# Kernel optimization log

Measured on AMD Instinct MI355X. Metric: run time of the kernel, lower is better.

Reference implementation:

```python
import jax, jax.numpy as jnp
import numpy as np
from jax import lax

B, DIM, H, W = 32, 256, 56, 56
HID = 4 * DIM
EPS = 1e-6


def setup_inputs() -> dict:
    key = jax.random.key(0)
    ks = jax.random.split(key, 8)
    x = jax.random.normal(ks[0], (B, DIM, H, W), dtype=jnp.float32)
    # depthwise conv: OIHW with feature_group_count=DIM -> [DIM, 1, 7, 7]
    conv_w = jax.random.normal(ks[1], (DIM, 1, 7, 7), dtype=jnp.float32) * 0.05
    conv_b = jax.random.normal(ks[2], (DIM,), dtype=jnp.float32) * 0.01
    ln_g = jnp.ones((DIM,), dtype=jnp.float32)
    ln_b = jnp.zeros((DIM,), dtype=jnp.float32)
    w1 = jax.random.normal(ks[3], (DIM, HID), dtype=jnp.float32) * (1.0 / np.sqrt(DIM))
    b1 = jax.random.normal(ks[4], (HID,), dtype=jnp.float32) * 0.01
    w2 = jax.random.normal(ks[5], (HID, DIM), dtype=jnp.float32) * (1.0 / np.sqrt(HID))
    b2 = jax.random.normal(ks[6], (DIM,), dtype=jnp.float32) * 0.01
    return {"x": x, "conv_w": conv_w, "conv_b": conv_b, "ln_g": ln_g,
            "ln_b": ln_b, "w1": w1, "b1": b1, "w2": w2, "b2": b2}


def reference(x, conv_w, conv_b, ln_g, ln_b, w1, b1, w2, b2):
    dim = x.shape[1]
    # 7x7 depthwise conv, stride 1, padding 3 (NCHW)
    y = lax.conv_general_dilated(
        x, conv_w, window_strides=(1, 1), padding=((3, 3), (3, 3)),
        dimension_numbers=("NCHW", "OIHW", "NCHW"), feature_group_count=dim)
    y = y + conv_b[None, :, None, None]
    # permute to NHWC
    y = jnp.transpose(y, (0, 2, 3, 1))  # [B, H, W, C]
    # LayerNorm over channel (last) dim, eps=1e-6, affine
    mu = jnp.mean(y, axis=-1, keepdims=True)
    var = jnp.mean(jnp.square(y - mu), axis=-1, keepdims=True)
    y = (y - mu) * lax.rsqrt(var + EPS) * ln_g + ln_b
    # MLP: Linear -> exact GELU -> Linear
    h = jax.nn.gelu(jnp.einsum("bhwc,cf->bhwf", y, w1) + b1, approximate=False)
    y = jnp.einsum("bhwf,fc->bhwc", h, w2) + b2
    # permute back to NCHW; stochastic depth is identity at eval time
    return jnp.transpose(y, (0, 3, 1, 2))
```

## Files before the change

kernel.cpp:

```cpp
#include <hip/hip_runtime.h>
#include <math.h>

#define CDIM 256
#define HW 3136
#define HID 1024

typedef __attribute__((ext_vector_type(4))) float f32x4;
typedef __attribute__((ext_vector_type(8))) short bf16x8;
typedef __attribute__((ext_vector_type(4))) short bf16x4;

__device__ __forceinline__ unsigned short f2bf(float f){
  unsigned int u = __float_as_uint(f);
  u += 0x7FFFu + ((u >> 16) & 1u);
  return (unsigned short)(u >> 16);
}

__device__ __forceinline__ void load_lds16(const void* g, void* l){
  __builtin_amdgcn_global_load_lds(
      (const __attribute__((address_space(1))) unsigned int*)g,
      (__attribute__((address_space(3))) unsigned int*)l, 16, 0, 0);
}

__global__ __launch_bounds__(256) void prep_kernel(
    const float* __restrict__ w1, const float* __restrict__ w2,
    unsigned short* __restrict__ w1t, unsigned short* __restrict__ w2t){
  __shared__ unsigned short sh[64][70];
  int blk = blockIdx.x;
  const float* src; unsigned short* dst; int M, N, tm, tn;
  if (blk < 64){ src = w1; dst = w1t; M = 256;  N = 1024; tm = blk >> 4; tn = blk & 15; }
  else { blk -= 64; src = w2; dst = w2t; M = 1024; N = 256;  tm = blk >> 2; tn = blk & 3; }
  const int t = threadIdx.x;

  {
    const int r = t >> 4, c4 = t & 15;
    #pragma unroll
    for (int rr = 0; rr < 4; ++rr){
      int row = rr * 16 + r;
      f32x4 v = *(const f32x4*)(src + (long)(tm * 64 + row) * N + tn * 64 + c4 * 4);
      #pragma unroll
      for (int k = 0; k < 4; ++k) sh[row][c4 * 4 + k] = f2bf(v[k]);
    }
  }
  __syncthreads();

  {
    const int n = t >> 2, seg = t & 3;
    bf16x8 o0, o1;
    #pragma unroll
    for (int j = 0; j < 8; ++j){
      o0[j] = (short)sh[seg * 16 + j][n];
      o1[j] = (short)sh[seg * 16 + 8 + j][n];
    }
    unsigned short* dp = dst + (long)(tn * 64 + n) * M + tm * 64 + seg * 16;
    *(bf16x8*)(dp) = o0;
    *(bf16x8*)(dp + 8) = o1;
  }
}

__global__ __launch_bounds__(256) void convln_kernel(
    const float* __restrict__ x, const float* __restrict__ cw,
    const float* __restrict__ cb, const float* __restrict__ lng,
    const float* __restrict__ lnb, unsigned short* __restrict__ y){
  __shared__ float tile[256 * 61];
  __shared__ float part_s[4][64];
  __shared__ float part_q[4][64];
  __shared__ float lg_s[256];
  __shared__ float lb_s[256];

  const int t = threadIdx.x;
  const int blk = blockIdx.x;
  const int b = blk / 56;
  const int h = blk - b * 56;
  const int c = t;

  lg_s[t] = lng[t];
  lb_s[t] = lnb[t];

  float acc[56];
  {
    float bias = cb[c];
    #pragma unroll
    for (int w = 0; w < 56; ++w) acc[w] = bias;
  }

  const float* xim = x + (long)(b * 256 + c) * HW;
  const float* cwc = cw + c * 49;
  for (int i = 0; i < 7; ++i){
    int hh = h - 3 + i;
    if (hh >= 0 && hh < 56){
      float seg[62];
      seg[0] = seg[1] = seg[2] = 0.f;
      seg[59] = seg[60] = seg[61] = 0.f;
      const float* xrow = xim + hh * 56;
      #pragma unroll
      for (int w4 = 0; w4 < 14; ++w4){
        f32x4 v = *(const f32x4*)(xrow + w4 * 4);
        seg[3 + w4 * 4 + 0] = v[0];
        seg[3 + w4 * 4 + 1] = v[1];
        seg[3 + w4 * 4 + 2] = v[2];
        seg[3 + w4 * 4 + 3] = v[3];
      }
      float wt7[7];
      #pragma unroll
      for (int j = 0; j < 7; ++j) wt7[j] = cwc[i * 7 + j];
      #pragma unroll
      for (int j = 0; j < 7; ++j){
        float wj = wt7[j];
        #pragma unroll
        for (int w = 0; w < 56; ++w)
          acc[w] = fmaf(seg[w + j], wj, acc[w]);
      }
    }
  }

  #pragma unroll
  for (int p = 0; p < 56; ++p) tile[c * 61 + p] = acc[p];
  __syncthreads();

  {
    int p = t & 63; if (p > 55) p = 55;
    const int q = t >> 6;
    float s = 0.f, qq = 0.f;
    #pragma unroll 8
    for (int j = 0; j < 64; ++j){
      float v = tile[(q * 64 + j) * 61 + p];
      s += v; qq = fmaf(v, v, qq);
    }
    part_s[q][p] = s;
    part_q[q][p] = qq;
  }
  __syncthreads();

  if (t < 224){
    const int p = t >> 2, c0 = (t & 3) * 64;
    float S = part_s[0][p] + part_s[1][p] + part_s[2][p] + part_s[3][p];
    float Q = part_q[0][p] + part_q[1][p] + part_q[2][p] + part_q[3][p];
    float mu = S * (1.0f / 256.0f);
    float var = Q * (1.0f / 256.0f) - mu * mu;
    float rs = rsqrtf(var + 1e-6f);
    long pos = (long)blk * 56 + p;
    int m7 = (int)(pos & 7);
    unsigned short* yp = y + pos * 256 + c0;
    #pragma unroll
    for (int j = 0; j < 8; ++j){
      bf16x8 o;
      #pragma unroll
      for (int k = 0; k < 8; ++k){
        int cc = c0 + j * 8 + k;
        float v = tile[cc * 61 + p];
        o[k] = (short)f2bf((v - mu) * rs * lg_s[cc] + lb_s[cc]);
      }
      *(bf16x8*)(yp + (j ^ m7) * 8) = o;
    }
  }
}

#define LDS_H0 32768
#define MLP_LDS (32768 + 18432)

__global__ __launch_bounds__(256, 3) void mlp_kernel(
    const unsigned short* __restrict__ y, const unsigned short* __restrict__ w1t,
    const unsigned short* __restrict__ w2t, const float* __restrict__ b1,
    const float* __restrict__ b2, float* __restrict__ out){
  __shared__ __align__(16) unsigned char smem[MLP_LDS];
  const int t = threadIdx.x;
  const int wv = t >> 6, lane = t & 63;
  const int lr = lane & 15, lq = lane >> 4;
  const int r7 = lr & 7;
  const int blk = blockIdx.x;

  {
    const unsigned char* ybase = (const unsigned char*)(y + (long)blk * 64 * 256);
    #pragma unroll
    for (int r = 0; r < 8; ++r){
      int g = wv * 8 + r;
      load_lds16(ybase + g * 1024 + lane * 16, smem + g * 1024);
    }
  }

  f32x4 acc2[4][4];
  #pragma unroll
  for (int a = 0; a < 4; ++a)
    #pragma unroll
    for (int bb = 0; bb < 4; ++bb) acc2[a][bb] = (f32x4){0.f, 0.f, 0.f, 0.f};

  __syncthreads();

  for (int ch = 0; ch < 16; ++ch){
    unsigned char* Hbuf = smem + LDS_H0 + (ch & 1) * 9216;

    const unsigned short* w1p = w1t + (((long)ch * 64 + wv * 16 + lr) << 8);
    bf16x8 wf[8];
    #pragma unroll
    for (int ks = 0; ks < 8; ++ks)
      wf[ks] = *(const bf16x8*)(w1p + ks * 32 + lq * 8);

    f32x4 acc1[4];
    #pragma unroll
    for (int mt = 0; mt < 4; ++mt) acc1[mt] = (f32x4){0.f, 0.f, 0.f, 0.f};
    #pragma unroll
    for (int ks = 0; ks < 8; ++ks){
      bf16x8 yf[4];
      #pragma unroll
      for (int mt = 0; mt < 4; ++mt){
        int jl = ks * 4 + lq;
        int ofs = (mt * 16 + lr) * 512 + (((jl & 24) | ((jl ^ r7) & 7)) << 4);
        yf[mt] = *(const bf16x8*)(smem + ofs);
      }
      #pragma unroll
      for (int mt = 0; mt < 4; ++mt)
        acc1[mt] = __builtin_amdgcn_mfma_f32_16x16x32_bf16(wf[ks], yf[mt], acc1[mt], 0, 0, 0);
    }

    bf16x8 w2f[2][4];
    #pragma unroll
    for (int ks2 = 0; ks2 < 2; ++ks2)
      #pragma unroll
      for (int ct = 0; ct < 4; ++ct)
        w2f[ks2][ct] = *(const bf16x8*)(w2t + (long)(wv * 64 + ct * 16 + lr) * 1024
                                        + ch * 64 + ks2 * 32 + lq * 8);

    {
      f32x4 bv = *(const f32x4*)(b1 + ch * 64 + wv * 16 + lq * 4);
      #pragma unroll
      for (int mt = 0; mt < 4; ++mt){
        bf16x4 hv;
        #pragma unroll
        for (int r = 0; r < 4; ++r){
          float pv = acc1[mt][r] + bv[r];
          float p2 = pv * pv;
          float u  = pv * fmaf(0.044715f, p2, 1.0f);
          float e  = __builtin_amdgcn_exp2f(-2.3022083f * u);
          float gl = pv * __builtin_amdgcn_rcpf(1.0f + e);
          hv[r] = (short)f2bf(gl);
        }
        *(bf16x4*)(Hbuf + (mt * 16 + lr) * 144 + wv * 32 + lq * 8) = hv;
      }
    }
    __syncthreads();

    #pragma unroll
    for (int ks2 = 0; ks2 < 2; ++ks2){
      bf16x8 hf[4];
      #pragma unroll
      for (int mt = 0; mt < 4; ++mt)
        hf[mt] = *(const bf16x8*)(Hbuf + (mt * 16 + lr) * 144 + ks2 * 64 + lq * 16);
      #pragma unroll
      for (int ct = 0; ct < 4; ++ct)
        #pragma unroll
        for (int mt = 0; mt < 4; ++mt)
          acc2[ct][mt] = __builtin_amdgcn_mfma_f32_16x16x32_bf16(w2f[ks2][ct], hf[mt], acc2[ct][mt], 0, 0, 0);
    }
  }

  #pragma unroll
  for (int ct = 0; ct < 4; ++ct){
    int cb = wv * 64 + ct * 16 + lq * 4;
    f32x4 b2v = *(const f32x4*)(b2 + cb);
    #pragma unroll
    for (int mt = 0; mt < 4; ++mt){
      int m = mt * 16 + lr;
      unsigned pos = (unsigned)(blk * 64 + m);
      unsigned bimg = pos / 3136u;
      unsigned hw = pos - bimg * 3136u;
      float* op = out + ((long)bimg * 256 + cb) * 3136 + hw;
      #pragma unroll
      for (int r = 0; r < 4; ++r)
        op[r * 3136] = acc2[ct][mt][r] + b2v[r];
    }
  }
}

extern "C" void kernel_launch(void* const* d_in, const int* in_sizes, int n_in,
                              void* d_out, int out_size, void* d_ws, size_t ws_size,
                              hipStream_t stream){
  const float* x  = (const float*)d_in[0];
  const float* cw = (const float*)d_in[1];
  const float* cb = (const float*)d_in[2];
  const float* lg = (const float*)d_in[3];
  const float* lb = (const float*)d_in[4];
  const float* w1 = (const float*)d_in[5];
  const float* b1 = (const float*)d_in[6];
  const float* w2 = (const float*)d_in[7];
  const float* b2 = (const float*)d_in[8];
  float* out = (float*)d_out;

  unsigned short* y   = (unsigned short*)d_ws;
  unsigned short* w1t = (unsigned short*)((char*)d_ws + 51380224);
  unsigned short* w2t = (unsigned short*)((char*)d_ws + 51904512);

  hipLaunchKernelGGL(prep_kernel,   dim3(128),  dim3(256), 0, stream, w1, w2, w1t, w2t);
  hipLaunchKernelGGL(convln_kernel, dim3(1792), dim3(256), 0, stream, x, cw, cb, lg, lb, y);
  hipLaunchKernelGGL(mlp_kernel,    dim3(1568), dim3(256), 0, stream, y, w1t, w2t, b1, b2, out);
}
```

Measured before the change: 527.5 us.

## Stage conv rows through LDS and single-buffer swizzled MLP hidden tile

The conv kernel now loads each input row for all 256 channels into LDS cooperatively with coalesced 16-byte loads, and each thread reads its channel's row from LDS. Before, each thread loaded its own strided channel row straight from global memory. The MLP kernel replaces its padded double-buffered hidden tile with a single XOR-swizzled 8KB buffer. This lowers LDS use so four blocks can fit per CU instead of three, at the cost of an extra barrier per chunk. The conv path also gains two barriers per kernel row.

```diff
diff --git a/kernel.cpp b/kernel.cpp
--- a/kernel.cpp
+++ b/kernel.cpp
@@ -61,7 +61,7 @@
     const float* __restrict__ x, const float* __restrict__ cw,
     const float* __restrict__ cb, const float* __restrict__ lng,
     const float* __restrict__ lnb, unsigned short* __restrict__ y){
-  __shared__ float tile[256 * 61];
+  __shared__ float buf[256 * 61];
   __shared__ float part_s[4][64];
   __shared__ float part_q[4][64];
   __shared__ float lg_s[256];
@@ -83,22 +83,34 @@
     for (int w = 0; w < 56; ++w) acc[w] = bias;
   }
 
-  const float* xim = x + (long)(b * 256 + c) * HW;
+  const int sl = t & 15;
+  const int rg = t >> 4;
+  const float* xb = x + (long)b * 256 * HW;
   const float* cwc = cw + c * 49;
+
   for (int i = 0; i < 7; ++i){
     int hh = h - 3 + i;
     if (hh >= 0 && hh < 56){
+      __syncthreads();
+      if (sl < 14){
+        #pragma unroll 4
+        for (int k = 0; k < 16; ++k){
+          int cr = k * 16 + rg;
+          f32x4 v = *(const f32x4*)(xb + (long)cr * HW + hh * 56 + sl * 4);
+          *(f32x4*)(buf + cr * 57 + sl * 4) = v;
+        }
+      }
+      __syncthreads();
       float seg[62];
       seg[0] = seg[1] = seg[2] = 0.f;
       seg[59] = seg[60] = seg[61] = 0.f;
-      const float* xrow = xim + hh * 56;
-      #pragma unroll
-      for (int w4 = 0; w4 < 14; ++w4){
-        f32x4 v = *(const f32x4*)(xrow + w4 * 4);
-        seg[3 + w4 * 4 + 0] = v[0];
-        seg[3 + w4 * 4 + 1] = v[1];
-        seg[3 + w4 * 4 + 2] = v[2];
-        seg[3 + w4 * 4 + 3] = v[3];
+      #pragma unroll
+      for (int s4 = 0; s4 < 14; ++s4){
+        f32x4 v = *(const f32x4*)(buf + c * 57 + s4 * 4);
+        seg[3 + s4 * 4 + 0] = v[0];
+        seg[3 + s4 * 4 + 1] = v[1];
+        seg[3 + s4 * 4 + 2] = v[2];
+        seg[3 + s4 * 4 + 3] = v[3];
       }
       float wt7[7];
       #pragma unroll
@@ -113,8 +125,9 @@
     }
   }
 
+  __syncthreads();
   #pragma unroll
-  for (int p = 0; p < 56; ++p) tile[c * 61 + p] = acc[p];
+  for (int p = 0; p < 56; ++p) buf[c * 61 + p] = acc[p];
   __syncthreads();
 
   {
@@ -123,7 +136,7 @@
     float s = 0.f, qq = 0.f;
     #pragma unroll 8
     for (int j = 0; j < 64; ++j){
-      float v = tile[(q * 64 + j) * 61 + p];
+      float v = buf[(q * 64 + j) * 61 + p];
       s += v; qq = fmaf(v, v, qq);
     }
     part_s[q][p] = s;
@@ -147,7 +160,7 @@
       #pragma unroll
       for (int k = 0; k < 8; ++k){
         int cc = c0 + j * 8 + k;
-        float v = tile[cc * 61 + p];
+        float v = buf[cc * 61 + p];
         o[k] = (short)f2bf((v - mu) * rs * lg_s[cc] + lb_s[cc]);
       }
       *(bf16x8*)(yp + (j ^ m7) * 8) = o;
@@ -156,9 +169,9 @@
 }
 
 #define LDS_H0 32768
-#define MLP_LDS (32768 + 18432)
-
-__global__ __launch_bounds__(256, 3) void mlp_kernel(
+#define MLP_LDS (32768 + 8192)
+
+__global__ __launch_bounds__(256, 4) void mlp_kernel(
     const unsigned short* __restrict__ y, const unsigned short* __restrict__ w1t,
     const unsigned short* __restrict__ w2t, const float* __restrict__ b1,
     const float* __restrict__ b2, float* __restrict__ out){
@@ -168,6 +181,7 @@
   const int lr = lane & 15, lq = lane >> 4;
   const int r7 = lr & 7;
   const int blk = blockIdx.x;
+  unsigned char* Hbuf = smem + LDS_H0;
 
   {
     const unsigned char* ybase = (const unsigned char*)(y + (long)blk * 64 * 256);
@@ -187,8 +201,6 @@
   __syncthreads();
 
   for (int ch = 0; ch < 16; ++ch){
-    unsigned char* Hbuf = smem + LDS_H0 + (ch & 1) * 9216;
-
     const unsigned short* w1p = w1t + (((long)ch * 64 + wv * 16 + lr) << 8);
     bf16x8 wf[8];
     #pragma unroll
@@ -222,6 +234,8 @@
 
     {
       f32x4 bv = *(const f32x4*)(b1 + ch * 64 + wv * 16 + lq * 4);
+      const int j = wv * 2 + (lq >> 1);
+      const int half = lq & 1;
       #pragma unroll
       for (int mt = 0; mt < 4; ++mt){
         bf16x4 hv;
@@ -234,7 +248,8 @@
           float gl = pv * __builtin_amdgcn_rcpf(1.0f + e);
           hv[r] = (short)f2bf(gl);
         }
-        *(bf16x4*)(Hbuf + (mt * 16 + lr) * 144 + wv * 32 + lq * 8) = hv;
+        int off = (mt * 16 + lr) * 128 + (((j ^ r7)) << 4) + (half << 3);
+        *(bf16x4*)(Hbuf + off) = hv;
       }
     }
     __syncthreads();
@@ -243,14 +258,17 @@
     for (int ks2 = 0; ks2 < 2; ++ks2){
       bf16x8 hf[4];
       #pragma unroll
-      for (int mt = 0; mt < 4; ++mt)
-        hf[mt] = *(const bf16x8*)(Hbuf + (mt * 16 + lr) * 144 + ks2 * 64 + lq * 16);
+      for (int mt = 0; mt < 4; ++mt){
+        int off = (mt * 16 + lr) * 128 + (((ks2 * 4 + lq) ^ r7) << 4);
+        hf[mt] = *(const bf16x8*)(Hbuf + off);
+      }
       #pragma unroll
       for (int ct = 0; ct < 4; ++ct)
         #pragma unroll
         for (int mt = 0; mt < 4; ++mt)
           acc2[ct][mt] = __builtin_amdgcn_mfma_f32_16x16x32_bf16(w2f[ks2][ct], hf[mt], acc2[ct][mt], 0, 0, 0);
     }
+    __syncthreads();
   }
 
   #pragma unroll
```

Result: slower. 546.0 us (+3.5%).
